# Optimization experiments

Hardware: AMD Instinct MI355X
Metric: run time of the kernel (lower is better)

## Reference

```python
import jax, jax.numpy as jnp
import numpy as np

NUM_HEADS = 16


def setup_inputs() -> dict:
    key = jax.random.key(0)
    ks = jax.random.split(key, 7)
    B, S, H = 4, 2048, 1024
    scale = 1.0 / np.sqrt(H)
    return {
        "hidden_states": jax.random.normal(ks[0], (B, S, H), dtype=jnp.float32),
        "attention_mask": jnp.ones((B, S), dtype=jnp.int32),
        "Wq": jax.random.normal(ks[1], (H, H), dtype=jnp.float32) * scale,
        "bq": jnp.zeros((H,), dtype=jnp.float32),
        "Wk": jax.random.normal(ks[2], (H, H), dtype=jnp.float32) * scale,
        "bk": jnp.zeros((H,), dtype=jnp.float32),
        "Wv": jax.random.normal(ks[3], (H, H), dtype=jnp.float32) * scale,
        "bv": jnp.zeros((H,), dtype=jnp.float32),
    }


def _split_heads(x, n_heads):
    B, S, H = x.shape
    return x.reshape(B, S, n_heads, H // n_heads).transpose(0, 2, 1, 3)  # [B,h,S,d]


def reference(hidden_states, attention_mask, Wq, bq, Wk, bk, Wv, bv):
    B, S, H = hidden_states.shape
    dh = H // NUM_HEADS
    # nn.Linear applies x @ W.T + b
    q = _split_heads(hidden_states @ Wq.T + bq, NUM_HEADS)
    k = _split_heads(hidden_states @ Wk.T + bk, NUM_HEADS)
    v = _split_heads(hidden_states @ Wv.T + bv, NUM_HEADS)
    scores = jnp.einsum("bhqd,bhkd->bhqk", q, k)  # [B,h,S,S]
    # masked_fill with -inf before scaling == masking after scaling
    mask = attention_mask[:, None, None, :] == 0
    scores = jnp.where(mask, -jnp.inf, scores)
    probs = jax.nn.softmax(scores / jnp.sqrt(jnp.float32(dh)), axis=-1)
    out = jnp.einsum("bhqk,bhkd->bhqd", probs, v)  # [B,h,S,d]
    return out.transpose(0, 2, 1, 3).reshape(B, S, H)
```

## Files before the change

kernel.cpp:

```cpp
#include <hip/hip_runtime.h>
#include <hip/hip_bf16.h>
#include <stdint.h>

constexpr int CB  = 4;
constexpr int CS  = 2048;
constexpr int CH  = 1024;
constexpr int CNH = 16;
constexpr int CDH = 64;
constexpr int CM  = CB * CS;

typedef __bf16 bf16x8 __attribute__((ext_vector_type(8)));
typedef float  f32x4  __attribute__((ext_vector_type(4)));

__device__ __forceinline__ unsigned short f2bf(float f) {
    union { float f; unsigned u; } c; c.f = f;
    unsigned u = c.u;
    unsigned r = (u + 0x7fffu + ((u >> 16) & 1u)) >> 16;
    return (unsigned short)r;
}

__device__ __forceinline__ void gl_lds16(const void* g, void* l) {
    __builtin_amdgcn_global_load_lds((const __attribute__((address_space(1))) uint32_t*)g,
                                     (__attribute__((address_space(3))) uint32_t*)l,
                                     16, 0, 0);
}

__device__ __forceinline__ float fexp2(float x) {
#if __has_builtin(__builtin_amdgcn_exp2f)
    return __builtin_amdgcn_exp2f(x);
#else
    return exp2f(x);
#endif
}

constexpr float C_SC = 0.125f * 1.44269504f;

__global__ __launch_bounds__(256) void cvt_all(const float* __restrict__ hs,
                                               const float* __restrict__ w0,
                                               const float* __restrict__ w1,
                                               const float* __restrict__ w2,
                                               unsigned short* __restrict__ Xb,
                                               unsigned short* __restrict__ Wb) {
    int z = blockIdx.y;
    const float* src; unsigned short* dst; int n4;
    if (z == 0)      { src = hs; dst = Xb;              n4 = CM * CH / 4; }
    else if (z == 1) { src = w0; dst = Wb;              n4 = CH * CH / 4; }
    else if (z == 2) { src = w1; dst = Wb + CH * CH;    n4 = CH * CH / 4; }
    else             { src = w2; dst = Wb + 2 * CH * CH; n4 = CH * CH / 4; }
    int i = blockIdx.x * blockDim.x + threadIdx.x;
    if (i < n4) {
        float4 v = ((const float4*)src)[i];
        ushort4 o;
        o.x = f2bf(v.x); o.y = f2bf(v.y); o.z = f2bf(v.z); o.w = f2bf(v.w);
        ((ushort4*)dst)[i] = o;
    }
}

__global__ __launch_bounds__(256) void qkv_gemm(
    const unsigned short* __restrict__ Xb,
    const unsigned short* __restrict__ Wb,
    const float* __restrict__ bq, const float* __restrict__ bk, const float* __restrict__ bv,
    unsigned short* __restrict__ Qo,
    unsigned short* __restrict__ Ko,
    unsigned short* __restrict__ Vt)
{
    __shared__ alignas(16) unsigned short As[2][128][32];
    __shared__ alignas(16) unsigned short Bs[2][128][32];
    const int tid  = threadIdx.x;
    const int wave = tid >> 6, lane = tid & 63;
    const int wm = wave >> 1, wn = wave & 1;
    const int col = lane & 15, quad = lane >> 4;
    const int gm = blockIdx.x * 128, gn = blockIdx.y * 128;
    const int z  = blockIdx.z;
    const unsigned short* W = Wb + (size_t)z * CH * CH;

    f32x4 zero = {0.f, 0.f, 0.f, 0.f};
    f32x4 acc[4][4];
    for (int i = 0; i < 4; i++) for (int j = 0; j < 4; j++) acc[i][j] = zero;

    const int arow = lane >> 2;
    const int acol = (lane & 3) * 8;

    auto stage = [&](int buf, int k0) {
        for (int c = 0; c < 2; ++c) {
            int r0 = wave * 32 + c * 16;
            gl_lds16(Xb + (size_t)(gm + r0 + arow) * CH + k0 + acol, &As[buf][r0][0]);
            gl_lds16(W  + (size_t)(gn + r0 + arow) * CH + k0 + acol, &Bs[buf][r0][0]);
        }
    };

    stage(0, 0);
    for (int kk = 0; kk < 32; ++kk) {
        int cur = kk & 1;
        __syncthreads();
        if (kk < 31) stage(cur ^ 1, (kk + 1) * 32);
        bf16x8 af[4], bfm[4];
        for (int i = 0; i < 4; i++)
            af[i] = *(const bf16x8*)&As[cur][wm * 64 + i * 16 + col][quad * 8];
        for (int j = 0; j < 4; j++)
            bfm[j] = *(const bf16x8*)&Bs[cur][wn * 64 + j * 16 + col][quad * 8];
        for (int i = 0; i < 4; i++)
            for (int j = 0; j < 4; j++)
                acc[i][j] = __builtin_amdgcn_mfma_f32_16x16x32_bf16(af[i], bfm[j], acc[i][j], 0, 0, 0);
    }

    const float* bias = (z == 0) ? bq : (z == 1) ? bk : bv;
    const float mulf = (z == 0) ? C_SC : 1.0f;
    unsigned short* dst01 = (z == 0) ? Qo : Ko;
    for (int j = 0; j < 4; j++) {
        int n = gn + wn * 64 + j * 16 + col;
        float bias_v = bias[n];
        int h = n >> 6, d = n & 63;
        for (int i = 0; i < 4; i++) {
            int m0 = gm + wm * 64 + i * 16 + quad * 4;
            int bb = m0 >> 11, ss = m0 & 2047;
            if (z == 2) {
                ushort4 pk;
                pk.x = f2bf(acc[i][j][0] + bias_v);
                pk.y = f2bf(acc[i][j][1] + bias_v);
                pk.z = f2bf(acc[i][j][2] + bias_v);
                pk.w = f2bf(acc[i][j][3] + bias_v);
                *(ushort4*)(Vt + ((size_t)(bb * CNH + h) * CDH + d) * CS + ss) = pk;
            } else {
                for (int r = 0; r < 4; r++) {
                    float v = (acc[i][j][r] + bias_v) * mulf;
                    dst01[((size_t)(bb * CNH + h) * CS + ss + r) * CDH + d] = f2bf(v);
                }
            }
        }
    }
}

__global__ __launch_bounds__(256, 3) void flash_attn(
    const unsigned short* __restrict__ Q,
    const unsigned short* __restrict__ K,
    const unsigned short* __restrict__ Vt,
    const int* __restrict__ mask,
    float* __restrict__ out)
{
    __shared__ alignas(16) unsigned short Ks[2][64][64];
    __shared__ alignas(16) unsigned short Vs[2][64][64];
    __shared__ alignas(16) unsigned short Ps[4][32][64];
    __shared__ unsigned int Mbits[64];

    const int tid  = threadIdx.x;
    const int wave = tid >> 6, lane = tid & 63;
    const int col = lane & 15, quad = lane >> 4;
    const int bh = blockIdx.y;
    const int bI = bh >> 4, hI = bh & 15;
    const int q0 = blockIdx.x * 128 + wave * 32;

    const unsigned short* Qp = Q  + (size_t)bh * CS * CDH;
    const unsigned short* Kp = K  + (size_t)bh * CS * CDH;
    const unsigned short* Vp = Vt + (size_t)bh * CDH * CS;

    {
        const int* mg = mask + bI * CS;
        for (int j = 0; j < 8; j++) {
            int idx = wave * 512 + j * 64 + lane;
            unsigned long long bal = __ballot(mg[idx] != 0);
            if (lane == 0) {
                Mbits[wave * 16 + j * 2]     = (unsigned int)bal;
                Mbits[wave * 16 + j * 2 + 1] = (unsigned int)(bal >> 32);
            }
        }
    }

    bf16x8 aq[2][2];
    for (int i = 0; i < 2; i++)
        for (int ks = 0; ks < 2; ks++)
            aq[i][ks] = *(const bf16x8*)(Qp + (size_t)(q0 + i * 16 + col) * CDH + ks * 32 + quad * 8);

    bf16x8 onesb;
    {
        union { unsigned short u; __bf16 b; } ob; ob.u = 0x3F80;
        for (int j = 0; j < 8; j++) onesb[j] = ob.b;
    }

    f32x4 zero = {0.f, 0.f, 0.f, 0.f};
    f32x4 o[2][4], lfr[2];
    for (int i = 0; i < 2; i++) {
        lfr[i] = zero;
        for (int id = 0; id < 4; id++) o[i][id] = zero;
    }

    const int srow = lane >> 3;
    const int schk = (lane & 7) ^ srow;

    auto stageKV = [&](int buf, int t) {
        const unsigned short* kg = Kp + (size_t)t * 64 * CDH;
        for (int c = 0; c < 2; c++) {
            int r0 = wave * 16 + c * 8;
            gl_lds16(kg + (size_t)(r0 + srow) * CDH + schk * 8, &Ks[buf][r0][0]);
            gl_lds16(Vp + (size_t)(r0 + srow) * CS + t * 64 + schk * 8, &Vs[buf][r0][0]);
        }
    };

    stageKV(0, 0);
    for (int kt = 0; kt < 32; ++kt) {
        int cur = kt & 1;
        __syncthreads();
        if (kt < 31) stageKV(cur ^ 1, kt + 1);

        f32x4 sfr[2][4];
        for (int i = 0; i < 2; i++) for (int ik = 0; ik < 4; ik++) sfr[i][ik] = zero;
        for (int ks = 0; ks < 2; ks++) {
            bf16x8 bkf[4];
            for (int ik = 0; ik < 4; ik++)
                bkf[ik] = *(const bf16x8*)&Ks[cur][ik * 16 + col][((ks * 4 + quad) ^ (col & 7)) * 8];
            for (int i = 0; i < 2; i++)
                for (int ik = 0; ik < 4; ik++)
                    sfr[i][ik] = __builtin_amdgcn_mfma_f32_16x16x32_bf16(aq[i][ks], bkf[ik], sfr[i][ik], 0, 0, 0);
        }

        unsigned int w0 = Mbits[kt * 2], w1 = Mbits[kt * 2 + 1];
        if ((w0 & w1) != 0xFFFFFFFFu) {
            float madd[4];
            madd[0] = ((w0 >> col) & 1u)        ? 0.f : -1.0e30f;
            madd[1] = ((w0 >> (col + 16)) & 1u) ? 0.f : -1.0e30f;
            madd[2] = ((w1 >> col) & 1u)        ? 0.f : -1.0e30f;
            madd[3] = ((w1 >> (col + 16)) & 1u) ? 0.f : -1.0e30f;
            for (int i = 0; i < 2; i++)
                for (int ik = 0; ik < 4; ik++)
                    for (int r = 0; r < 4; r++)
                        sfr[i][ik][r] += madd[ik];
        }

        for (int i = 0; i < 2; i++)
            for (int ik = 0; ik < 4; ik++)
                for (int r = 0; r < 4; r++) {
                    float p = fexp2(sfr[i][ik][r]);
                    union { float f; unsigned u; } cu; cu.f = p;
                    int row = i * 16 + quad * 4 + r;
                    int slot = (ik * 2 + (col >> 3)) ^ (row & 7);
                    Ps[wave][row][slot * 8 + (col & 7)] = (unsigned short)(cu.u >> 16);
                }

        for (int ks = 0; ks < 2; ks++) {
            bf16x8 ap[2], bvf[4];
            for (int i = 0; i < 2; i++)
                ap[i] = *(const bf16x8*)&Ps[wave][i * 16 + col][((ks * 4 + quad) ^ (col & 7)) * 8];
            for (int id = 0; id < 4; id++)
                bvf[id] = *(const bf16x8*)&Vs[cur][id * 16 + col][((ks * 4 + quad) ^ (col & 7)) * 8];
            for (int i = 0; i < 2; i++) {
                for (int id = 0; id < 4; id++)
                    o[i][id] = __builtin_amdgcn_mfma_f32_16x16x32_bf16(ap[i], bvf[id], o[i][id], 0, 0, 0);
                lfr[i] = __builtin_amdgcn_mfma_f32_16x16x32_bf16(ap[i], onesb, lfr[i], 0, 0, 0);
            }
        }
    }

    for (int i = 0; i < 2; i++)
        for (int r = 0; r < 4; r++) {
            int sI = q0 + i * 16 + quad * 4 + r;
            float inv = 1.0f / lfr[i][r];
            for (int id = 0; id < 4; id++)
                out[((size_t)(bI * CS + sI)) * CH + hI * CDH + id * 16 + col] = o[i][id][r] * inv;
        }
}

extern "C" void kernel_launch(void* const* d_in, const int* in_sizes, int n_in,
                              void* d_out, int out_size, void* d_ws, size_t ws_size,
                              hipStream_t stream) {
    const float* hs  = (const float*)d_in[0];
    const int*  mask = (const int*)d_in[1];
    const float* Wq  = (const float*)d_in[2];
    const float* bq  = (const float*)d_in[3];
    const float* Wk  = (const float*)d_in[4];
    const float* bk  = (const float*)d_in[5];
    const float* Wv  = (const float*)d_in[6];
    const float* bv  = (const float*)d_in[7];
    float* out = (float*)d_out;

    char* ws = (char*)d_ws;
    unsigned short* Xb = (unsigned short*)(ws);
    unsigned short* Wb = (unsigned short*)(ws + 16777216);
    unsigned short* Qb = (unsigned short*)(ws + 23068672);
    unsigned short* Kb = (unsigned short*)(ws + 39845888);
    unsigned short* Vt = (unsigned short*)(ws + 56623104);

    cvt_all<<<dim3(8192, 4), 256, 0, stream>>>(hs, Wq, Wk, Wv, Xb, Wb);

    qkv_gemm<<<dim3(CM / 128, CH / 128, 3), 256, 0, stream>>>(Xb, Wb, bq, bk, bv, Qb, Kb, Vt);

    flash_attn<<<dim3(CS / 128, CB * CNH), 256, 0, stream>>>(Qb, Kb, Vt, mask, out);
}
```

Before: 277.5 us.

## Stage QKV epilogue through LDS and double query rows per attention wave

The QKV GEMM epilogue now writes bias-added bf16 results into a shared-memory tile and then emits coalesced 16-byte stores to Q, K and transposed V, replacing scattered 2-byte and 8-byte stores. The flash-attention kernel gives each wave 64 query rows instead of 32, so every K/V tile loaded into LDS is reused across twice as many queries, and the grid shrinks to 256-row blocks. P values are packed in pairs with v_perm into dword LDS writes and unpacked on read. The larger per-wave tile raises register pressure (launch bounds drop to 2 blocks per SM) and halves the number of attention blocks, which may reduce occupancy and latency hiding.

```diff
diff --git a/kernel.cpp b/kernel.cpp
--- a/kernel.cpp
+++ b/kernel.cpp
@@ -31,6 +31,23 @@
 #else
     return exp2f(x);
 #endif
+}
+
+__device__ __forceinline__ unsigned vperm(unsigned s0, unsigned s1, unsigned sel) {
+#if __has_builtin(__builtin_amdgcn_perm)
+    return __builtin_amdgcn_perm(s0, s1, sel);
+#else
+    unsigned r = 0;
+    for (int k = 0; k < 4; k++) {
+        unsigned idx = (sel >> (8 * k)) & 0xff;
+        unsigned byte = (idx < 4) ? (s1 >> (8 * idx)) : (s0 >> (8 * (idx - 4)));
+        r |= (byte & 0xff) << (8 * k);
+    }
+    return r;
+#endif
+}
+__device__ __forceinline__ unsigned pack_hihalf(unsigned lo_u, unsigned hi_u) {
+    return vperm(hi_u, lo_u, 0x07060302u);
 }
 
 constexpr float C_SC = 0.125f * 1.44269504f;
@@ -64,8 +81,13 @@
     unsigned short* __restrict__ Ko,
     unsigned short* __restrict__ Vt)
 {
-    __shared__ alignas(16) unsigned short As[2][128][32];
-    __shared__ alignas(16) unsigned short Bs[2][128][32];
+    __shared__ alignas(16) unsigned char smem[34816];
+    typedef unsigned short (*tile_t)[128][32];
+    tile_t As = (tile_t)smem;
+    tile_t Bs = (tile_t)(smem + 16384);
+    typedef unsigned short (*ep_t)[136];
+    ep_t Ep = (ep_t)smem;
+
     const int tid  = threadIdx.x;
     const int wave = tid >> 6, lane = tid & 63;
     const int wm = wave >> 1, wn = wave & 1;
@@ -104,34 +126,58 @@
                 acc[i][j] = __builtin_amdgcn_mfma_f32_16x16x32_bf16(af[i], bfm[j], acc[i][j], 0, 0, 0);
     }
 
+    __syncthreads();
+
     const float* bias = (z == 0) ? bq : (z == 1) ? bk : bv;
-    const float mulf = (z == 0) ? C_SC : 1.0f;
-    unsigned short* dst01 = (z == 0) ? Qo : Ko;
-    for (int j = 0; j < 4; j++) {
-        int n = gn + wn * 64 + j * 16 + col;
-        float bias_v = bias[n];
-        int h = n >> 6, d = n & 63;
-        for (int i = 0; i < 4; i++) {
-            int m0 = gm + wm * 64 + i * 16 + quad * 4;
-            int bb = m0 >> 11, ss = m0 & 2047;
-            if (z == 2) {
-                ushort4 pk;
-                pk.x = f2bf(acc[i][j][0] + bias_v);
-                pk.y = f2bf(acc[i][j][1] + bias_v);
-                pk.z = f2bf(acc[i][j][2] + bias_v);
-                pk.w = f2bf(acc[i][j][3] + bias_v);
-                *(ushort4*)(Vt + ((size_t)(bb * CNH + h) * CDH + d) * CS + ss) = pk;
-            } else {
+    const int bb = gm >> 11, ss0 = gm & 2047;
+    const int h0 = gn >> 6;
+
+    if (z == 2) {
+        for (int j = 0; j < 4; j++) {
+            int nl = wn * 64 + j * 16 + col;
+            float bias_v = bias[gn + nl];
+            for (int i = 0; i < 4; i++) {
+                int ml = wm * 64 + i * 16 + quad * 4;
+                unsigned d0 = (unsigned)f2bf(acc[i][j][0] + bias_v) |
+                              ((unsigned)f2bf(acc[i][j][1] + bias_v) << 16);
+                unsigned d1 = (unsigned)f2bf(acc[i][j][2] + bias_v) |
+                              ((unsigned)f2bf(acc[i][j][3] + bias_v) << 16);
+                *(unsigned*)&Ep[nl][ml]     = d0;
+                *(unsigned*)&Ep[nl][ml + 2] = d1;
+            }
+        }
+        __syncthreads();
+        for (int p = 0; p < 8; p++) {
+            int nl = p * 16 + (tid >> 4);
+            int seg = tid & 15;
+            uint4 v = *(const uint4*)&Ep[nl][seg * 8];
+            int h = h0 + (nl >> 6), d = nl & 63;
+            *(uint4*)(Vt + ((size_t)(bb * CNH + h) * CDH + d) * CS + ss0 + seg * 8) = v;
+        }
+    } else {
+        const float mulf = (z == 0) ? C_SC : 1.0f;
+        for (int j = 0; j < 4; j++) {
+            int nl = wn * 64 + j * 16 + col;
+            float bias_v = bias[gn + nl];
+            for (int i = 0; i < 4; i++)
                 for (int r = 0; r < 4; r++) {
-                    float v = (acc[i][j][r] + bias_v) * mulf;
-                    dst01[((size_t)(bb * CNH + h) * CS + ss + r) * CDH + d] = f2bf(v);
+                    int ml = wm * 64 + i * 16 + quad * 4 + r;
+                    Ep[ml][nl] = f2bf((acc[i][j][r] + bias_v) * mulf);
                 }
-            }
-        }
-    }
-}
-
-__global__ __launch_bounds__(256, 3) void flash_attn(
+        }
+        __syncthreads();
+        unsigned short* dst01 = (z == 0) ? Qo : Ko;
+        for (int p = 0; p < 8; p++) {
+            int ml = p * 16 + (tid >> 4);
+            int half = (tid >> 3) & 1, seg = tid & 7;
+            uint4 v = *(const uint4*)&Ep[ml][half * 64 + seg * 8];
+            int h = h0 + half;
+            *(uint4*)(dst01 + ((size_t)(bb * CNH + h) * CS + ss0 + ml) * CDH + seg * 8) = v;
+        }
+    }
+}
+
+__global__ __launch_bounds__(256, 2) void flash_attn(
     const unsigned short* __restrict__ Q,
     const unsigned short* __restrict__ K,
     const unsigned short* __restrict__ Vt,
@@ -140,7 +186,7 @@
 {
     __shared__ alignas(16) unsigned short Ks[2][64][64];
     __shared__ alignas(16) unsigned short Vs[2][64][64];
-    __shared__ alignas(16) unsigned short Ps[4][32][64];
+    __shared__ alignas(16) unsigned int   Ps[4][64][32];
     __shared__ unsigned int Mbits[64];
 
     const int tid  = threadIdx.x;
@@ -148,7 +194,7 @@
     const int col = lane & 15, quad = lane >> 4;
     const int bh = blockIdx.y;
     const int bI = bh >> 4, hI = bh & 15;
-    const int q0 = blockIdx.x * 128 + wave * 32;
+    const int q0 = blockIdx.x * 256 + wave * 64;
 
     const unsigned short* Qp = Q  + (size_t)bh * CS * CDH;
     const unsigned short* Kp = K  + (size_t)bh * CS * CDH;
@@ -166,8 +212,8 @@
         }
     }
 
-    bf16x8 aq[2][2];
-    for (int i = 0; i < 2; i++)
+    bf16x8 aq[4][2];
+    for (int i = 0; i < 4; i++)
         for (int ks = 0; ks < 2; ks++)
             aq[i][ks] = *(const bf16x8*)(Qp + (size_t)(q0 + i * 16 + col) * CDH + ks * 32 + quad * 8);
 
@@ -178,8 +224,8 @@
     }
 
     f32x4 zero = {0.f, 0.f, 0.f, 0.f};
-    f32x4 o[2][4], lfr[2];
-    for (int i = 0; i < 2; i++) {
+    f32x4 o[4][4], lfr[4];
+    for (int i = 0; i < 4; i++) {
         lfr[i] = zero;
         for (int id = 0; id < 4; id++) o[i][id] = zero;
     }
@@ -202,13 +248,13 @@
         __syncthreads();
         if (kt < 31) stageKV(cur ^ 1, kt + 1);
 
-        f32x4 sfr[2][4];
-        for (int i = 0; i < 2; i++) for (int ik = 0; ik < 4; ik++) sfr[i][ik] = zero;
+        f32x4 sfr[4][4];
+        for (int i = 0; i < 4; i++) for (int ik = 0; ik < 4; ik++) sfr[i][ik] = zero;
         for (int ks = 0; ks < 2; ks++) {
             bf16x8 bkf[4];
             for (int ik = 0; ik < 4; ik++)
                 bkf[ik] = *(const bf16x8*)&Ks[cur][ik * 16 + col][((ks * 4 + quad) ^ (col & 7)) * 8];
-            for (int i = 0; i < 2; i++)
+            for (int i = 0; i < 4; i++)
                 for (int ik = 0; ik < 4; ik++)
                     sfr[i][ik] = __builtin_amdgcn_mfma_f32_16x16x32_bf16(aq[i][ks], bkf[ik], sfr[i][ik], 0, 0, 0);
         }
@@ -220,37 +266,50 @@
             madd[1] = ((w0 >> (col + 16)) & 1u) ? 0.f : -1.0e30f;
             madd[2] = ((w1 >> col) & 1u)        ? 0.f : -1.0e30f;
             madd[3] = ((w1 >> (col + 16)) & 1u) ? 0.f : -1.0e30f;
-            for (int i = 0; i < 2; i++)
+            for (int i = 0; i < 4; i++)
                 for (int ik = 0; ik < 4; ik++)
                     for (int r = 0; r < 4; r++)
                         sfr[i][ik][r] += madd[ik];
         }
 
-        for (int i = 0; i < 2; i++)
-            for (int ik = 0; ik < 4; ik++)
+        for (int i = 0; i < 4; i++)
+            for (int ik = 0; ik < 2; ik++)
                 for (int r = 0; r < 4; r++) {
-                    float p = fexp2(sfr[i][ik][r]);
-                    union { float f; unsigned u; } cu; cu.f = p;
+                    union { float f; unsigned u; } a, b;
+                    a.f = fexp2(sfr[i][ik][r]);
+                    b.f = fexp2(sfr[i][ik + 2][r]);
+                    unsigned dw = pack_hihalf(a.u, b.u);
                     int row = i * 16 + quad * 4 + r;
-                    int slot = (ik * 2 + (col >> 3)) ^ (row & 7);
-                    Ps[wave][row][slot * 8 + (col & 7)] = (unsigned short)(cu.u >> 16);
+                    int p = ik * 16 + col;
+                    Ps[wave][row][(((p >> 2) ^ (row & 7)) << 2) + (p & 3)] = dw;
                 }
 
-        for (int ks = 0; ks < 2; ks++) {
-            bf16x8 ap[2], bvf[4];
-            for (int i = 0; i < 2; i++)
-                ap[i] = *(const bf16x8*)&Ps[wave][i * 16 + col][((ks * 4 + quad) ^ (col & 7)) * 8];
-            for (int id = 0; id < 4; id++)
-                bvf[id] = *(const bf16x8*)&Vs[cur][id * 16 + col][((ks * 4 + quad) ^ (col & 7)) * 8];
-            for (int i = 0; i < 2; i++) {
+        for (int i = 0; i < 4; i++) {
+            const unsigned* base = &Ps[wave][i * 16 + col][0];
+            uint4 w0v = *(const uint4*)(base + (((quad * 2 + 0) ^ (col & 7)) << 2));
+            uint4 w1v = *(const uint4*)(base + (((quad * 2 + 1) ^ (col & 7)) << 2));
+            uint4 lo, hi;
+            lo.x = vperm(w0v.y, w0v.x, 0x05040100u); hi.x = vperm(w0v.y, w0v.x, 0x07060302u);
+            lo.y = vperm(w0v.w, w0v.z, 0x05040100u); hi.y = vperm(w0v.w, w0v.z, 0x07060302u);
+            lo.z = vperm(w1v.y, w1v.x, 0x05040100u); hi.z = vperm(w1v.y, w1v.x, 0x07060302u);
+            lo.w = vperm(w1v.w, w1v.z, 0x05040100u); hi.w = vperm(w1v.w, w1v.z, 0x07060302u);
+            bf16x8 ap0, ap1;
+            __builtin_memcpy(&ap0, &lo, 16);
+            __builtin_memcpy(&ap1, &hi, 16);
+
+            for (int ks = 0; ks < 2; ks++) {
+                bf16x8 ap = (ks == 0) ? ap0 : ap1;
+                bf16x8 bvf[4];
                 for (int id = 0; id < 4; id++)
-                    o[i][id] = __builtin_amdgcn_mfma_f32_16x16x32_bf16(ap[i], bvf[id], o[i][id], 0, 0, 0);
-                lfr[i] = __builtin_amdgcn_mfma_f32_16x16x32_bf16(ap[i], onesb, lfr[i], 0, 0, 0);
+                    bvf[id] = *(const bf16x8*)&Vs[cur][id * 16 + col][((ks * 4 + quad) ^ (col & 7)) * 8];
+                for (int id = 0; id < 4; id++)
+                    o[i][id] = __builtin_amdgcn_mfma_f32_16x16x32_bf16(ap, bvf[id], o[i][id], 0, 0, 0);
+                lfr[i] = __builtin_amdgcn_mfma_f32_16x16x32_bf16(ap, onesb, lfr[i], 0, 0, 0);
             }
         }
     }
 
-    for (int i = 0; i < 2; i++)
+    for (int i = 0; i < 4; i++)
         for (int r = 0; r < 4; r++) {
             int sI = q0 + i * 16 + quad * 4 + r;
             float inv = 1.0f / lfr[i][r];
@@ -283,5 +342,5 @@
 
     qkv_gemm<<<dim3(CM / 128, CH / 128, 3), 256, 0, stream>>>(Xb, Wb, bq, bk, bv, Qb, Kb, Vt);
 
-    flash_attn<<<dim3(CS / 128, CB * CNH), 256, 0, stream>>>(Qb, Kb, Vt, mask, out);
-}
+    flash_attn<<<dim3(CS / 256, CB * CNH), 256, 0, stream>>>(Qb, Kb, Vt, mask, out);
+}
```

Measured after the change: 261.6 us. 1.06x faster.
